# Optimization experiments

Hardware: AMD Instinct MI355X
Metric: run time of the kernel (lower is better)

## Reference

```python
import math
import jax, jax.numpy as jnp
import numpy as np

N_ATOMS = 500000
N_TYPES = 16
N_FEAT = 64
N_CENTER = 40000
N_NEIGH = 6
H1, H2 = 128, 64
CUTOFF = 3.5
D_IN = 3 + 3 * N_FEAT  # 195

# static off-diagonal (j,k) pairs, row-major == torch's ~eye boolean mask order
_JJ, _KK = np.nonzero(~np.eye(N_NEIGH, dtype=bool))


def setup_inputs() -> dict:
    key = jax.random.key(0)
    ks = jax.random.split(key, 9)
    atoms_xyz = jax.random.normal(ks[0], (N_ATOMS, 3), dtype=jnp.float32) * 5.0
    atom_type_idx = jax.random.randint(ks[1], (N_ATOMS,), 0, N_TYPES)
    embed_table = jax.random.normal(ks[2], (N_TYPES, N_FEAT), dtype=jnp.float32)
    atom_i_idx = jax.random.randint(ks[3], (N_CENTER,), 0, N_ATOMS)
    # distinct neighbor indices per row (real neighbor lists never repeat an atom)
    base = jax.random.randint(ks[4], (N_CENTER, 1), 0, N_ATOMS)
    atom_j_idx = (base + jnp.arange(N_NEIGH)) % N_ATOMS
    # center->neighbor distances, strictly positive (within angular cutoff scale)
    dist_ij = 0.5 + 3.0 * jax.random.uniform(ks[5], (N_CENTER, N_NEIGH), dtype=jnp.float32)
    W1 = jax.random.normal(ks[6], (H1, D_IN), dtype=jnp.float32) / np.sqrt(D_IN).astype(np.float32)
    b1 = jnp.zeros((H1,), dtype=jnp.float32)
    W2 = jax.random.normal(ks[7], (H2, H1), dtype=jnp.float32) / np.sqrt(H1).astype(np.float32)
    b2 = jnp.zeros((H2,), dtype=jnp.float32)
    return dict(atoms_xyz=atoms_xyz, embed_table=embed_table, dist_ij=dist_ij,
                W1=W1, b1=b1, W2=W2, b2=b2,
                atom_type_idx=atom_type_idx, atom_i_idx=atom_i_idx, atom_j_idx=atom_j_idx)


def _ang_input(atoms_xyz, embed_table, dist_ij, atom_type_idx, atom_i_idx, atom_j_idx):
    # Build angular descriptor directly on off-diagonal (j,k) triples -> [C, T, 3+3F]
    xyz_j = atoms_xyz[atom_j_idx]                       # [C, N, 3]
    diff = xyz_j[:, _JJ] - xyz_j[:, _KK]                # [C, T, 3]
    d_jk = jnp.sqrt(jnp.sum(diff * diff, axis=-1))      # [C, T]
    dij = dist_ij[:, _JJ]                                # [C, T]
    dik = dist_ij[:, _KK]
    mx = jnp.maximum(dij, dik)
    mn = jnp.minimum(dij, dik)
    d_jk_norm = (d_jk - mx + mn) / (2.0 * mn)
    e_i = embed_table[atom_type_idx[atom_i_idx]]        # [C, F]
    e_n = embed_table[atom_type_idx[atom_j_idx]]        # [C, N, F]
    e_j = e_n[:, _JJ]                                    # [C, T, F]
    e_k = e_n[:, _KK]
    ang = jnp.concatenate([
        dij[..., None], dik[..., None], d_jk_norm[..., None],
        jnp.broadcast_to(e_i[:, None, :], e_j.shape),
        e_j / dij[..., None],
        e_k / dik[..., None],
    ], axis=-1)                                          # [C, T, 3+3F]
    return ang


def reference(atoms_xyz, embed_table, dist_ij, W1, b1, W2, b2,
              atom_type_idx, atom_i_idx, atom_j_idx):
    ang = _ang_input(atoms_xyz, embed_table, dist_ij,
                     atom_type_idx, atom_i_idx, atom_j_idx)   # [C, T, D_IN]
    C, T, _ = ang.shape
    x = ang.reshape(-1, D_IN)
    x = jax.nn.celu(x @ W1.T + b1)
    x = jax.nn.celu(x @ W2.T + b2)
    out = x.reshape(C, T, H2)
    # smooth angular cutoff from the ij, ik distance columns
    fc = 0.5 * jnp.cos(math.pi * jnp.clip(ang[:, :, 0:2] / CUTOFF, 0.0, 1.0)) + 0.5
    fc = jnp.prod(fc, axis=-1, keepdims=True)            # [C, T, 1]
    desc = jnp.sum(out * fc, axis=1)                     # [C, H2]
    return desc
```

## Files before the change

kernel.cpp:

```cpp
#include <hip/hip_runtime.h>
#include <hip/hip_bf16.h>

typedef __attribute__((ext_vector_type(8))) short bfrag;
typedef __attribute__((ext_vector_type(4))) float facc;
typedef __attribute__((ext_vector_type(4))) int ivec4;
typedef __attribute__((ext_vector_type(2))) int ivec2;
typedef __attribute__((ext_vector_type(4))) short svec4;

#define DIN 195
#define H1 128
#define H2 64
#define CPB 4
#define ROWS 128
#define TPB 512
#define X1STR 136
#define VSTR 72

#define W1T_ELEMS (8*7*64*8)
#define W2T_ELEMS (4*4*64*8)

__device__ __forceinline__ short f2bf(float v) {
    __hip_bfloat16 h = __float2bfloat16(v);
    return __builtin_bit_cast(short, h);
}
__device__ __forceinline__ float celu1(float v) {
    return v > 0.f ? v : (__expf(v) - 1.f);
}

__global__ void prep_weights(const float* __restrict__ W1, const float* __restrict__ W2,
                             const float* __restrict__ b1,
                             __hip_bfloat16* __restrict__ W1t, __hip_bfloat16* __restrict__ W2t) {
    int i = blockIdx.x * 256 + threadIdx.x;
    if (i < W1T_ELEMS) {
        int e = i & 7, l = (i >> 3) & 63;
        int k0 = (i >> 9) % 7, mt = (i >> 9) / 7;
        int h = mt * 16 + (l & 15);
        int kp = k0 * 32 + ((l >> 4) & 3) * 8 + e;
        float v = 0.f;
        if (kp < 192)       v = W1[h * DIN + 3 + kp];
        else if (kp < 195)  v = W1[h * DIN + (kp - 192)];
        else if (kp == 195) v = b1[h];
        W1t[i] = __float2bfloat16(v);
    } else {
        int j = i - W1T_ELEMS;
        if (j < W2T_ELEMS) {
            int e = j & 7, l = (j >> 3) & 63;
            int k0 = (j >> 9) & 3, nt = j >> 11;
            int h = nt * 16 + (l & 15);
            int k = k0 * 32 + ((l >> 4) & 3) * 8 + e;
            W2t[j] = __float2bfloat16(W2[h * H1 + k]);
        }
    }
}

template<bool PREP>
__global__ __launch_bounds__(TPB, 8) void angnet(
    const float* __restrict__ atoms_xyz,
    const float* __restrict__ embed,
    const float* __restrict__ dist_ij,
    const float* __restrict__ b1,
    const float* __restrict__ b2,
    const int* __restrict__ atype,
    const int* __restrict__ aidx,
    const int* __restrict__ ajdx,
    const __hip_bfloat16* __restrict__ W1t,
    const __hip_bfloat16* __restrict__ W2t,
    const float* __restrict__ W1f,
    const float* __restrict__ W2f,
    float* __restrict__ out)
{
    __shared__ __align__(16) __hip_bfloat16 x1s[ROWS][X1STR];
    __shared__ __align__(16) __hip_bfloat16 vst[CPB][7][VSTR];
    __shared__ __align__(16) __hip_bfloat16 tvp[512];
    __shared__ __hip_bfloat16 fcs[ROWS];

    float* stg  = (float*)&x1s[0][0];
    int*   tidxp = (int*)(stg + 96);

    const int tid = threadIdx.x;
    const int C0 = blockIdx.x * CPB;

    if (tid < 64) {
        ivec4 zz = {0, 0, 0, 0};
        ((ivec4*)tvp)[tid] = zz;
    } else if (tid >= 64 && tid < 92) {
        int q = tid - 64, c = q / 7, r = q % 7;
        tidxp[c * 7 + r] = (r == 6) ? atype[aidx[C0 + c]] : atype[ajdx[(C0 + c) * 6 + r]];
    } else if (tid >= 96 && tid < 168) {
        int q = tid - 96, c = q / 18, rr = q % 18, n = rr / 3, ax = rr % 3;
        stg[c * 18 + n * 3 + ax] = atoms_xyz[(long)ajdx[(C0 + c) * 6 + n] * 3 + ax];
    } else if (tid >= 168 && tid < 192) {
        int q = tid - 168, c = q / 6, n = q % 6;
        stg[72 + c * 6 + n] = dist_ij[(C0 + c) * 6 + n];
    }
    __syncthreads();

    if (tid < CPB * 7 * 8) {
        int c = tid / 56, rem = tid % 56, v = rem / 8, ch = rem % 8;
        int ti = tidxp[c * 7 + v];
        float sc = (v < 6) ? (1.0f / stg[72 + c * 6 + v]) : 1.0f;
        const float* ep = &embed[ti * 64 + ch * 8];
        float4 e0 = *(const float4*)ep;
        float4 e1 = *(const float4*)(ep + 4);
        bfrag t;
        t[0] = f2bf(e0.x * sc); t[1] = f2bf(e0.y * sc);
        t[2] = f2bf(e0.z * sc); t[3] = f2bf(e0.w * sc);
        t[4] = f2bf(e1.x * sc); t[5] = f2bf(e1.y * sc);
        t[6] = f2bf(e1.z * sc); t[7] = f2bf(e1.w * sc);
        *(bfrag*)&vst[c][v][ch * 8] = t;
    } else if (tid >= 256 && tid < 256 + CPB * 30) {
        int q = tid - 256, c = q / 30, t = q % 30;
        int j = t / 5, k2 = t - j * 5, k = k2 + (k2 >= j ? 1 : 0);
        float dij = stg[72 + c * 6 + j], dik = stg[72 + c * 6 + k];
        float dx = stg[c * 18 + j * 3 + 0] - stg[c * 18 + k * 3 + 0];
        float dy = stg[c * 18 + j * 3 + 1] - stg[c * 18 + k * 3 + 1];
        float dz = stg[c * 18 + j * 3 + 2] - stg[c * 18 + k * 3 + 2];
        float djk = sqrtf(dx * dx + dy * dy + dz * dz);
        float mx = fmaxf(dij, dik), mn = fminf(dij, dik);
        float djkn = (djk - mx + mn) / (2.0f * mn);
        int r = c * 32 + t;
        svec4 pk;
        pk[0] = f2bf(dij); pk[1] = f2bf(dik); pk[2] = f2bf(djkn); pk[3] = f2bf(1.0f);
        *(svec4*)&tvp[r * 4] = pk;
        const float PIF = 3.14159265358979323846f;
        float ca = __cosf(PIF * (dij * (1.0f / 3.5f)));
        float cb = __cosf(PIF * (dik * (1.0f / 3.5f)));
        fcs[r] = __float2bfloat16((0.5f * ca + 0.5f) * (0.5f * cb + 0.5f));
    } else if (tid >= 376 && tid < 384) {
        int p = tid - 376;
        fcs[(p >> 1) * 32 + 30 + (p & 1)] = __float2bfloat16(0.f);
    }
    __syncthreads();

    const int w = tid >> 6, l = tid & 63, lr = l & 15, lq = l >> 4;

    int jA = lr / 5, k2A = lr % 5; int kA = k2A + (k2A >= jA ? 1 : 0);
    int tB = 16 + lr, jB = 0, kB = 0;
    if (tB < 30) { jB = tB / 5; int k2B = tB % 5; kB = k2B + (k2B >= jB ? 1 : 0); }
    const int joA = jA * VSTR, joB = jB * VSTR, koA = kA * VSTR, koB = kB * VSTR;
    const __hip_bfloat16* vb[4];
    #pragma unroll
    for (int c = 0; c < 4; ++c) vb[c] = &vst[c][0][lq * 8];

    facc a1[8];
    #pragma unroll
    for (int n = 0; n < 8; ++n) a1[n] = (facc){0.f, 0.f, 0.f, 0.f};

    #pragma unroll
    for (int k0 = 0; k0 < 7; ++k0) {
        bfrag Af;
        if (PREP) {
            Af = *(const bfrag*)&W1t[(w * 7 + k0) * 512 + l * 8];
        } else {
            #pragma unroll
            for (int e = 0; e < 8; ++e) {
                int kp = k0 * 32 + lq * 8 + e;
                int h = w * 16 + lr;
                float v = 0.f;
                if (kp < 192)       v = W1f[h * DIN + 3 + kp];
                else if (kp < 195)  v = W1f[h * DIN + kp - 192];
                else if (kp == 195) v = b1[h];
                Af[e] = f2bf(v);
            }
        }
        #pragma unroll
        for (int n = 0; n < 8; ++n) {
            bfrag Bf;
            if (k0 < 6) {
                const __hip_bfloat16* bp;
                if (k0 < 2)      bp = vb[n >> 1] + 6 * VSTR + (k0 & 1) * 32;
                else if (k0 < 4) bp = vb[n >> 1] + ((n & 1) ? joB : joA) + (k0 & 1) * 32;
                else             bp = vb[n >> 1] + ((n & 1) ? koB : koA) + (k0 & 1) * 32;
                Bf = *(const bfrag*)bp;
            } else {
                svec4 tv = *(const svec4*)&tvp[(n * 16 + lr) * 4];
                ivec2 ti = __builtin_bit_cast(ivec2, tv);
                int lo = (lq == 0) ? ti[0] : 0;
                int hi = (lq == 0) ? ti[1] : 0;
                ivec4 bi = {lo, hi, 0, 0};
                Bf = __builtin_bit_cast(bfrag, bi);
            }
            a1[n] = __builtin_amdgcn_mfma_f32_16x16x32_bf16(Af, Bf, a1[n], 0, 0, 0);
        }
    }

    #pragma unroll
    for (int n = 0; n < 8; ++n) {
        svec4 pk;
        #pragma unroll
        for (int g = 0; g < 4; ++g) pk[g] = f2bf(celu1(a1[n][g]));
        *(svec4*)&x1s[n * 16 + lr][w * 16 + lq * 4] = pk;
    }
    __syncthreads();

    facc a2[4];
    #pragma unroll
    for (int n = 0; n < 4; ++n) a2[n] = (facc){0.f, 0.f, 0.f, 0.f};

    #pragma unroll
    for (int k0 = 0; k0 < 4; ++k0) {
        bfrag Af2 = *(const bfrag*)&x1s[w * 16 + lr][k0 * 32 + lq * 8];
        #pragma unroll
        for (int n = 0; n < 4; ++n) {
            bfrag Bf2;
            if (PREP) {
                Bf2 = *(const bfrag*)&W2t[(n * 4 + k0) * 512 + l * 8];
            } else {
                #pragma unroll
                for (int e = 0; e < 8; ++e)
                    Bf2[e] = f2bf(W2f[(n * 16 + lr) * H1 + k0 * 32 + lq * 8 + e]);
            }
            a2[n] = __builtin_amdgcn_mfma_f32_16x16x32_bf16(Af2, Bf2, a2[n], 0, 0, 0);
        }
    }

    {
        float fr[4];
        #pragma unroll
        for (int g = 0; g < 4; ++g) fr[g] = __bfloat162float(fcs[w * 16 + lq * 4 + g]);
        float t[4];
        #pragma unroll
        for (int n = 0; n < 4; ++n) {
            float b2v = b2[n * 16 + lr];
            float s = 0.f;
            #pragma unroll
            for (int g = 0; g < 4; ++g)
                s += celu1(a2[n][g] + b2v) * fr[g];
            s += __shfl_xor(s, 16);
            s += __shfl_xor(s, 32);
            t[n] = s;
        }
        if (lq == 0) {
            #pragma unroll
            for (int n = 0; n < 4; ++n)
                tvp[w * 64 + n * 16 + lr] = __float2bfloat16(t[n]);
        }
    }
    __syncthreads();

    if (tid < 256) {
        int c = tid >> 6, o = tid & 63;
        out[(long)(C0 + c) * 64 + o] =
            __bfloat162float(tvp[(2 * c) * 64 + o]) + __bfloat162float(tvp[(2 * c + 1) * 64 + o]);
    }
}

extern "C" void kernel_launch(void* const* d_in, const int* in_sizes, int n_in,
                              void* d_out, int out_size, void* d_ws, size_t ws_size,
                              hipStream_t stream) {
    const float* atoms_xyz = (const float*)d_in[0];
    const float* embed     = (const float*)d_in[1];
    const float* dist_ij   = (const float*)d_in[2];
    const float* W1        = (const float*)d_in[3];
    const float* b1        = (const float*)d_in[4];
    const float* W2        = (const float*)d_in[5];
    const float* b2        = (const float*)d_in[6];
    const int*   atype     = (const int*)d_in[7];
    const int*   aidx      = (const int*)d_in[8];
    const int*   ajdx      = (const int*)d_in[9];
    float* out = (float*)d_out;

    const int n_center = in_sizes[8];
    const int n_blocks = n_center / CPB;

    size_t need = (size_t)(W1T_ELEMS + W2T_ELEMS) * sizeof(__hip_bfloat16);
    if (ws_size >= need) {
        __hip_bfloat16* W1t = (__hip_bfloat16*)d_ws;
        __hip_bfloat16* W2t = W1t + W1T_ELEMS;
        int prep_total = W1T_ELEMS + W2T_ELEMS;
        prep_weights<<<(prep_total + 255) / 256, 256, 0, stream>>>(W1, W2, b1, W1t, W2t);
        angnet<true><<<n_blocks, TPB, 0, stream>>>(atoms_xyz, embed, dist_ij, b1, b2,
                                                   atype, aidx, ajdx, W1t, W2t, W1, W2, out);
    } else {
        angnet<false><<<n_blocks, TPB, 0, stream>>>(atoms_xyz, embed, dist_ij, b1, b2,
                                                    atype, aidx, ajdx, nullptr, nullptr, W1, W2, out);
    }
}
```

Measured before the change: 119.2 us.

## Factor first layer into per-neighbor projections combined by a selection matmul

Rather than running the full 195-wide first-layer GEMM over all 30 (j,k) triples, the kernel first projects the center embedding and each neighbor's scaled embedding through the matching W1 column blocks once per atom. A second small MFMA then assembles each triple's hidden pre-activation from a 16-wide one-hot selection matrix that also carries the three distance features, with bias folded into the center term. This removes the redundant per-pair work in the first layer. The cost is an extra shared-memory staging step and barrier, plus bf16 rounding of the intermediate projections.

```diff
diff --git a/kernel.cpp b/kernel.cpp
--- a/kernel.cpp
+++ b/kernel.cpp
@@ -4,7 +4,6 @@
 typedef __attribute__((ext_vector_type(8))) short bfrag;
 typedef __attribute__((ext_vector_type(4))) float facc;
 typedef __attribute__((ext_vector_type(4))) int ivec4;
-typedef __attribute__((ext_vector_type(2))) int ivec2;
 typedef __attribute__((ext_vector_type(4))) short svec4;
 
 #define DIN 195
@@ -16,7 +15,8 @@
 #define X1STR 136
 #define VSTR 72
 
-#define W1T_ELEMS (8*7*64*8)
+#define W1A_ELEMS (3*2*8*64*8)
+#define W1C_ELEMS (128*4)
 #define W2T_ELEMS (4*4*64*8)
 
 __device__ __forceinline__ short f2bf(float v) {
@@ -28,21 +28,23 @@
 }
 
 __global__ void prep_weights(const float* __restrict__ W1, const float* __restrict__ W2,
-                             const float* __restrict__ b1,
-                             __hip_bfloat16* __restrict__ W1t, __hip_bfloat16* __restrict__ W2t) {
+                             __hip_bfloat16* __restrict__ W1A, __hip_bfloat16* __restrict__ W1C,
+                             __hip_bfloat16* __restrict__ W2t) {
     int i = blockIdx.x * 256 + threadIdx.x;
-    if (i < W1T_ELEMS) {
+    if (i < W1A_ELEMS) {
         int e = i & 7, l = (i >> 3) & 63;
-        int k0 = (i >> 9) % 7, mt = (i >> 9) / 7;
-        int h = mt * 16 + (l & 15);
-        int kp = k0 * 32 + ((l >> 4) & 3) * 8 + e;
-        float v = 0.f;
-        if (kp < 192)       v = W1[h * DIN + 3 + kp];
-        else if (kp < 195)  v = W1[h * DIN + (kp - 192)];
-        else if (kp == 195) v = b1[h];
-        W1t[i] = __float2bfloat16(v);
+        int ht = (i >> 9) & 7, k0 = (i >> 12) & 1, type = i >> 13;
+        int h = ht * 16 + (l & 15);
+        int kk = k0 * 32 + ((l >> 4) & 3) * 8 + e;
+        int base = (type == 0) ? 3 : (type == 1) ? 67 : 131;
+        W1A[i] = __float2bfloat16(W1[h * DIN + base + kk]);
+    } else if (i < W1A_ELEMS + W1C_ELEMS) {
+        int j = i - W1A_ELEMS;
+        int h = j >> 2, q = j & 3;
+        float v = (q < 3) ? W1[h * DIN + q] : 0.f;
+        W1C[j] = __float2bfloat16(v);
     } else {
-        int j = i - W1T_ELEMS;
+        int j = i - W1A_ELEMS - W1C_ELEMS;
         if (j < W2T_ELEMS) {
             int e = j & 7, l = (j >> 3) & 63;
             int k0 = (j >> 9) & 3, nt = j >> 11;
@@ -63,7 +65,8 @@
     const int* __restrict__ atype,
     const int* __restrict__ aidx,
     const int* __restrict__ ajdx,
-    const __hip_bfloat16* __restrict__ W1t,
+    const __hip_bfloat16* __restrict__ W1A,
+    const __hip_bfloat16* __restrict__ W1C,
     const __hip_bfloat16* __restrict__ W2t,
     const float* __restrict__ W1f,
     const float* __restrict__ W2f,
@@ -73,31 +76,33 @@
     __shared__ __align__(16) __hip_bfloat16 vst[CPB][7][VSTR];
     __shared__ __align__(16) __hip_bfloat16 tvp[512];
     __shared__ __hip_bfloat16 fcs[ROWS];
-
-    float* stg  = (float*)&x1s[0][0];
-    int*   tidxp = (int*)(stg + 96);
+    __shared__ float stg[96];
+    __shared__ int   tidxs[28];
+
+    __hip_bfloat16 (*bmat)[ROWS][16] = (__hip_bfloat16 (*)[ROWS][16])&x1s[0][0];
+    __hip_bfloat16 (*smat)[16]       = (__hip_bfloat16 (*)[16])((char*)&x1s[0][0] + 16384);
 
     const int tid = threadIdx.x;
     const int C0 = blockIdx.x * CPB;
 
-    if (tid < 64) {
+    if (tid < 28) {
+        int c = tid / 7, r = tid % 7;
+        tidxs[tid] = (r == 6) ? atype[aidx[C0 + c]] : atype[ajdx[(C0 + c) * 6 + r]];
+    } else if (tid >= 32 && tid < 104) {
+        int q = tid - 32, c = q / 18, rr = q % 18, n = rr / 3, ax = rr % 3;
+        stg[c * 18 + n * 3 + ax] = atoms_xyz[(long)ajdx[(C0 + c) * 6 + n] * 3 + ax];
+    } else if (tid >= 104 && tid < 128) {
+        int q = tid - 104, c = q / 6, n = q % 6;
+        stg[72 + c * 6 + n] = dist_ij[(C0 + c) * 6 + n];
+    } else if (tid == 192) {
         ivec4 zz = {0, 0, 0, 0};
-        ((ivec4*)tvp)[tid] = zz;
-    } else if (tid >= 64 && tid < 92) {
-        int q = tid - 64, c = q / 7, r = q % 7;
-        tidxp[c * 7 + r] = (r == 6) ? atype[aidx[C0 + c]] : atype[ajdx[(C0 + c) * 6 + r]];
-    } else if (tid >= 96 && tid < 168) {
-        int q = tid - 96, c = q / 18, rr = q % 18, n = rr / 3, ax = rr % 3;
-        stg[c * 18 + n * 3 + ax] = atoms_xyz[(long)ajdx[(C0 + c) * 6 + n] * 3 + ax];
-    } else if (tid >= 168 && tid < 192) {
-        int q = tid - 168, c = q / 6, n = q % 6;
-        stg[72 + c * 6 + n] = dist_ij[(C0 + c) * 6 + n];
+        *(ivec4*)&tvp[0] = zz;
     }
     __syncthreads();
 
     if (tid < CPB * 7 * 8) {
         int c = tid / 56, rem = tid % 56, v = rem / 8, ch = rem % 8;
-        int ti = tidxp[c * 7 + v];
+        int ti = tidxs[c * 7 + v];
         float sc = (v < 6) ? (1.0f / stg[72 + c * 6 + v]) : 1.0f;
         const float* ep = &embed[ti * 64 + ch * 8];
         float4 e0 = *(const float4*)ep;
@@ -108,88 +113,146 @@
         t[4] = f2bf(e1.x * sc); t[5] = f2bf(e1.y * sc);
         t[6] = f2bf(e1.z * sc); t[7] = f2bf(e1.w * sc);
         *(bfrag*)&vst[c][v][ch * 8] = t;
-    } else if (tid >= 256 && tid < 256 + CPB * 30) {
-        int q = tid - 256, c = q / 30, t = q % 30;
-        int j = t / 5, k2 = t - j * 5, k = k2 + (k2 >= j ? 1 : 0);
-        float dij = stg[72 + c * 6 + j], dik = stg[72 + c * 6 + k];
-        float dx = stg[c * 18 + j * 3 + 0] - stg[c * 18 + k * 3 + 0];
-        float dy = stg[c * 18 + j * 3 + 1] - stg[c * 18 + k * 3 + 1];
-        float dz = stg[c * 18 + j * 3 + 2] - stg[c * 18 + k * 3 + 2];
-        float djk = sqrtf(dx * dx + dy * dy + dz * dz);
-        float mx = fmaxf(dij, dik), mn = fminf(dij, dik);
-        float djkn = (djk - mx + mn) / (2.0f * mn);
-        int r = c * 32 + t;
-        svec4 pk;
-        pk[0] = f2bf(dij); pk[1] = f2bf(dik); pk[2] = f2bf(djkn); pk[3] = f2bf(1.0f);
-        *(svec4*)&tvp[r * 4] = pk;
-        const float PIF = 3.14159265358979323846f;
-        float ca = __cosf(PIF * (dij * (1.0f / 3.5f)));
-        float cb = __cosf(PIF * (dik * (1.0f / 3.5f)));
-        fcs[r] = __float2bfloat16((0.5f * ca + 0.5f) * (0.5f * cb + 0.5f));
-    } else if (tid >= 376 && tid < 384) {
-        int p = tid - 376;
-        fcs[(p >> 1) * 32 + 30 + (p & 1)] = __float2bfloat16(0.f);
+    } else if (tid >= 256 && tid < 384) {
+        int r = tid - 256;
+        int c = r >> 5, t = r & 31;
+        ivec4 zz = {0, 0, 0, 0};
+        *(ivec4*)&smat[r][0] = zz;
+        *(ivec4*)&smat[r][8] = zz;
+        if (t < 30) {
+            int j = t / 5, k2 = t - j * 5, k = k2 + (k2 >= j ? 1 : 0);
+            float dij = stg[72 + c * 6 + j], dik = stg[72 + c * 6 + k];
+            float dx = stg[c * 18 + j * 3 + 0] - stg[c * 18 + k * 3 + 0];
+            float dy = stg[c * 18 + j * 3 + 1] - stg[c * 18 + k * 3 + 1];
+            float dz = stg[c * 18 + j * 3 + 2] - stg[c * 18 + k * 3 + 2];
+            float djk = sqrtf(dx * dx + dy * dy + dz * dz);
+            float mx = fmaxf(dij, dik), mn = fminf(dij, dik);
+            float djkn = (djk - mx + mn) / (2.0f * mn);
+            short one = f2bf(1.0f);
+            smat[r][0] = __builtin_bit_cast(__hip_bfloat16, one);
+            smat[r][1 + j] = __builtin_bit_cast(__hip_bfloat16, one);
+            smat[r][7 + k] = __builtin_bit_cast(__hip_bfloat16, one);
+            smat[r][13] = __float2bfloat16(dij);
+            smat[r][14] = __float2bfloat16(dik);
+            smat[r][15] = __float2bfloat16(djkn);
+            const float PIF = 3.14159265358979323846f;
+            float ca = __cosf(PIF * (dij * (1.0f / 3.5f)));
+            float cb = __cosf(PIF * (dik * (1.0f / 3.5f)));
+            fcs[r] = __float2bfloat16((0.5f * ca + 0.5f) * (0.5f * cb + 0.5f));
+        } else {
+            fcs[r] = __float2bfloat16(0.f);
+        }
+    } else if (tid >= 384 && tid < 512) {
+        int h = tid - 384;
+        short wv[3];
+        if (PREP) {
+            svec4 wc = *(const svec4*)&W1C[h * 4];
+            wv[0] = wc[0]; wv[1] = wc[1]; wv[2] = wc[2];
+        } else {
+            wv[0] = f2bf(W1f[h * DIN + 0]);
+            wv[1] = f2bf(W1f[h * DIN + 1]);
+            wv[2] = f2bf(W1f[h * DIN + 2]);
+        }
+        #pragma unroll
+        for (int c = 0; c < 4; ++c) {
+            bmat[c][h][13] = __builtin_bit_cast(__hip_bfloat16, wv[0]);
+            bmat[c][h][14] = __builtin_bit_cast(__hip_bfloat16, wv[1]);
+            bmat[c][h][15] = __builtin_bit_cast(__hip_bfloat16, wv[2]);
+        }
     }
     __syncthreads();
 
     const int w = tid >> 6, l = tid & 63, lr = l & 15, lq = l >> 4;
 
-    int jA = lr / 5, k2A = lr % 5; int kA = k2A + (k2A >= jA ? 1 : 0);
-    int tB = 16 + lr, jB = 0, kB = 0;
-    if (tB < 30) { jB = tB / 5; int k2B = tB % 5; kB = k2B + (k2B >= jB ? 1 : 0); }
-    const int joA = jA * VSTR, joB = jB * VSTR, koA = kA * VSTR, koB = kB * VSTR;
-    const __hip_bfloat16* vb[4];
-    #pragma unroll
-    for (int c = 0; c < 4; ++c) vb[c] = &vst[c][0][lq * 8];
+    {
+        int rU = (lr < 4) ? lr : 0;
+        int offU = (rU * 7 + 6) * VSTR;
+        int cP0 = lr / 6, vP0 = lr - cP0 * 6;
+        int offP0 = (cP0 * 7 + vP0) * VSTR;
+        int r1 = 16 + lr; if (r1 > 23) r1 = 23;
+        int cP1 = r1 / 6, vP1 = r1 - cP1 * 6;
+        int offP1 = (cP1 * 7 + vP1) * VSTR;
+
+        facc accU = {0,0,0,0}, accP0 = {0,0,0,0}, accP1 = {0,0,0,0}, accQ0 = {0,0,0,0}, accQ1 = {0,0,0,0};
+        #pragma unroll
+        for (int k0 = 0; k0 < 2; ++k0) {
+            int ko = k0 * 32 + lq * 8;
+            bfrag fU  = *(const bfrag*)&((__hip_bfloat16*)vst)[offU + ko];
+            bfrag fP0 = *(const bfrag*)&((__hip_bfloat16*)vst)[offP0 + ko];
+            bfrag fP1 = *(const bfrag*)&((__hip_bfloat16*)vst)[offP1 + ko];
+            bfrag Wei, Wej, Wek;
+            if (PREP) {
+                Wei = *(const bfrag*)&W1A[((0 * 2 + k0) * 8 + w) * 512 + l * 8];
+                Wej = *(const bfrag*)&W1A[((1 * 2 + k0) * 8 + w) * 512 + l * 8];
+                Wek = *(const bfrag*)&W1A[((2 * 2 + k0) * 8 + w) * 512 + l * 8];
+            } else {
+                int h = w * 16 + lr;
+                #pragma unroll
+                for (int e = 0; e < 8; ++e) {
+                    int kk = k0 * 32 + lq * 8 + e;
+                    Wei[e] = f2bf(W1f[h * DIN + 3 + kk]);
+                    Wej[e] = f2bf(W1f[h * DIN + 67 + kk]);
+                    Wek[e] = f2bf(W1f[h * DIN + 131 + kk]);
+                }
+            }
+            accU  = __builtin_amdgcn_mfma_f32_16x16x32_bf16(fU,  Wei, accU,  0, 0, 0);
+            accP0 = __builtin_amdgcn_mfma_f32_16x16x32_bf16(fP0, Wej, accP0, 0, 0, 0);
+            accP1 = __builtin_amdgcn_mfma_f32_16x16x32_bf16(fP1, Wej, accP1, 0, 0, 0);
+            accQ0 = __builtin_amdgcn_mfma_f32_16x16x32_bf16(fP0, Wek, accQ0, 0, 0, 0);
+            accQ1 = __builtin_amdgcn_mfma_f32_16x16x32_bf16(fP1, Wek, accQ1, 0, 0, 0);
+        }
+
+        int h = w * 16 + lr;
+        if (lq == 0) {
+            float b1v = b1[h];
+            #pragma unroll
+            for (int g = 0; g < 4; ++g)
+                bmat[g][h][0] = __float2bfloat16(accU[g] + b1v);
+        }
+        #pragma unroll
+        for (int g = 0; g < 4; ++g) {
+            int row = lq * 4 + g;
+            int cg = row / 6, ng = row - cg * 6;
+            bmat[cg][h][1 + ng] = __float2bfloat16(accP0[g]);
+            bmat[cg][h][7 + ng] = __float2bfloat16(accQ0[g]);
+            int row1 = 16 + row;
+            if (row1 < 24) {
+                int c1 = row1 / 6, n1 = row1 - c1 * 6;
+                bmat[c1][h][1 + n1] = __float2bfloat16(accP1[g]);
+                bmat[c1][h][7 + n1] = __float2bfloat16(accQ1[g]);
+            }
+        }
+    }
+    __syncthreads();
 
     facc a1[8];
     #pragma unroll
     for (int n = 0; n < 8; ++n) a1[n] = (facc){0.f, 0.f, 0.f, 0.f};
-
-    #pragma unroll
-    for (int k0 = 0; k0 < 7; ++k0) {
-        bfrag Af;
-        if (PREP) {
-            Af = *(const bfrag*)&W1t[(w * 7 + k0) * 512 + l * 8];
-        } else {
+    {
+        const int cw = w >> 1;
+        const int r = w * 16 + lr;
+        const __hip_bfloat16* zp = &tvp[0];
+        const __hip_bfloat16* sp = (lq < 2) ? &smat[r][lq * 8] : zp;
+        bfrag Sf = *(const bfrag*)sp;
+        #pragma unroll
+        for (int n = 0; n < 8; ++n) {
+            int h = n * 16 + lr;
+            const __hip_bfloat16* ap = (lq < 2) ? &bmat[cw][h][lq * 8] : zp;
+            bfrag Af = *(const bfrag*)ap;
+            a1[n] = __builtin_amdgcn_mfma_f32_16x16x32_bf16(Af, Sf, a1[n], 0, 0, 0);
+        }
+    }
+    __syncthreads();
+
+    {
+        const int r = w * 16 + lr;
+        #pragma unroll
+        for (int n = 0; n < 8; ++n) {
+            svec4 pk;
             #pragma unroll
-            for (int e = 0; e < 8; ++e) {
-                int kp = k0 * 32 + lq * 8 + e;
-                int h = w * 16 + lr;
-                float v = 0.f;
-                if (kp < 192)       v = W1f[h * DIN + 3 + kp];
-                else if (kp < 195)  v = W1f[h * DIN + kp - 192];
-                else if (kp == 195) v = b1[h];
-                Af[e] = f2bf(v);
-            }
-        }
-        #pragma unroll
-        for (int n = 0; n < 8; ++n) {
-            bfrag Bf;
-            if (k0 < 6) {
-                const __hip_bfloat16* bp;
-                if (k0 < 2)      bp = vb[n >> 1] + 6 * VSTR + (k0 & 1) * 32;
-                else if (k0 < 4) bp = vb[n >> 1] + ((n & 1) ? joB : joA) + (k0 & 1) * 32;
-                else             bp = vb[n >> 1] + ((n & 1) ? koB : koA) + (k0 & 1) * 32;
-                Bf = *(const bfrag*)bp;
-            } else {
-                svec4 tv = *(const svec4*)&tvp[(n * 16 + lr) * 4];
-                ivec2 ti = __builtin_bit_cast(ivec2, tv);
-                int lo = (lq == 0) ? ti[0] : 0;
-                int hi = (lq == 0) ? ti[1] : 0;
-                ivec4 bi = {lo, hi, 0, 0};
-                Bf = __builtin_bit_cast(bfrag, bi);
-            }
-            a1[n] = __builtin_amdgcn_mfma_f32_16x16x32_bf16(Af, Bf, a1[n], 0, 0, 0);
-        }
-    }
-
-    #pragma unroll
-    for (int n = 0; n < 8; ++n) {
-        svec4 pk;
-        #pragma unroll
-        for (int g = 0; g < 4; ++g) pk[g] = f2bf(celu1(a1[n][g]));
-        *(svec4*)&x1s[n * 16 + lr][w * 16 + lq * 4] = pk;
+            for (int g = 0; g < 4; ++g) pk[g] = f2bf(celu1(a1[n][g]));
+            *(svec4*)&x1s[r][n * 16 + lq * 4] = pk;
+        }
     }
     __syncthreads();
 
@@ -263,16 +326,17 @@
     const int n_center = in_sizes[8];
     const int n_blocks = n_center / CPB;
 
-    size_t need = (size_t)(W1T_ELEMS + W2T_ELEMS) * sizeof(__hip_bfloat16);
+    size_t need = (size_t)(W1A_ELEMS + W1C_ELEMS + W2T_ELEMS) * sizeof(__hip_bfloat16);
     if (ws_size >= need) {
-        __hip_bfloat16* W1t = (__hip_bfloat16*)d_ws;
-        __hip_bfloat16* W2t = W1t + W1T_ELEMS;
-        int prep_total = W1T_ELEMS + W2T_ELEMS;
-        prep_weights<<<(prep_total + 255) / 256, 256, 0, stream>>>(W1, W2, b1, W1t, W2t);
+        __hip_bfloat16* W1Ap = (__hip_bfloat16*)d_ws;
+        __hip_bfloat16* W1Cp = W1Ap + W1A_ELEMS;
+        __hip_bfloat16* W2tp = W1Cp + W1C_ELEMS;
+        int prep_total = W1A_ELEMS + W1C_ELEMS + W2T_ELEMS;
+        prep_weights<<<(prep_total + 255) / 256, 256, 0, stream>>>(W1, W2, W1Ap, W1Cp, W2tp);
         angnet<true><<<n_blocks, TPB, 0, stream>>>(atoms_xyz, embed, dist_ij, b1, b2,
-                                                   atype, aidx, ajdx, W1t, W2t, W1, W2, out);
+                                                   atype, aidx, ajdx, W1Ap, W1Cp, W2tp, W1, W2, out);
     } else {
         angnet<false><<<n_blocks, TPB, 0, stream>>>(atoms_xyz, embed, dist_ij, b1, b2,
-                                                    atype, aidx, ajdx, nullptr, nullptr, W1, W2, out);
-    }
-}
+                                                    atype, aidx, ajdx, nullptr, nullptr, nullptr, W1, W2, out);
+    }
+}
```

Measured after the change: 128.9 us. 8.1% more time.
